# Performance work log

Measured on AMD Instinct MI355X. Metric: run time of the kernel, lower is better.

Reference implementation:

```python
import jax, jax.numpy as jnp
import numpy as np

B, S, D, H = 2, 2048, 1024, 16
DEPTH = D // H


def setup_inputs() -> dict:
    key = jax.random.key(0)
    ks = jax.random.split(key, 8)
    w_scale = 0.02
    # causal mask: 1.0 where attention is NOT allowed (added as mask * -1e9)
    causal = jnp.triu(jnp.ones((S, S), dtype=jnp.float32), k=1)[None, None]  # [1,1,S,S]
    return {
        "q": jax.random.normal(ks[0], (B, S, D), dtype=jnp.float32),
        "k": jax.random.normal(ks[1], (B, S, D), dtype=jnp.float32),
        "v": jax.random.normal(ks[2], (B, S, D), dtype=jnp.float32),
        "mask": causal,
        "Wq": jax.random.normal(ks[3], (D, D), dtype=jnp.float32) * w_scale,
        "bq": jnp.zeros((D,), dtype=jnp.float32),
        "Wk": jax.random.normal(ks[4], (D, D), dtype=jnp.float32) * w_scale,
        "bk": jnp.zeros((D,), dtype=jnp.float32),
        "Wv": jax.random.normal(ks[5], (D, D), dtype=jnp.float32) * w_scale,
        "bv": jnp.zeros((D,), dtype=jnp.float32),
        "Wo": jax.random.normal(ks[6], (D, D), dtype=jnp.float32) * w_scale,
        "bo": jnp.zeros((D,), dtype=jnp.float32),
    }


def _split_heads(x):
    # [B,S,D] -> [B,H,S,depth]
    return x.reshape(B, S, H, DEPTH).transpose(0, 2, 1, 3)


def reference(q, k, v, mask, Wq, bq, Wk, bk, Wv, bv, Wo, bo):
    qh = _split_heads(q @ Wq + bq)
    kh = _split_heads(k @ Wk + bk)
    vh = _split_heads(v @ Wv + bv)
    scale = 1.0 / jnp.sqrt(jnp.asarray(DEPTH, dtype=qh.dtype))
    logits = jnp.einsum('bhqd,bhkd->bhqk', qh, kh) * scale  # [B,H,S,S]
    logits = logits + mask * (-1e9)
    attn = jax.nn.softmax(logits, axis=-1)
    out = jnp.einsum('bhqk,bhkd->bhqd', attn, vh)  # [B,H,S,depth]
    out = out.transpose(0, 2, 1, 3).reshape(B, S, D)
    return out @ Wo + bo
```

## Files before the change

### kernel.cpp

```cpp
#include <hip/hip_runtime.h>


typedef unsigned short u16;
typedef unsigned int u32;

using bf16x8 = __attribute__((ext_vector_type(8))) short;
using bf16x4 = __attribute__((ext_vector_type(4))) short;
using f32x4  = __attribute__((ext_vector_type(4))) float;

#define SEQ 2048
#define DMODEL 1024
#define NHEAD 16
#define DEPTH 64
#define BATCH 2
#define M_ROWS (BATCH * SEQ)

__device__ __forceinline__ u16 f2bf(float f) {
    union { float f; u32 u; } v; v.f = f;
    u32 u = v.u;
    return (u16)((u + 0x7FFFu + ((u >> 16) & 1u)) >> 16);
}
__device__ __forceinline__ u16 f2bf_trunc(float f) {
    union { float f; u32 u; } v; v.f = f;
    return (u16)(v.u >> 16);
}

__device__ __forceinline__ f32x4 mfma16(bf16x8 a, bf16x8 b, f32x4 c) {
    return __builtin_amdgcn_mfma_f32_16x16x32_bf16(a, b, c, 0, 0, 0);
}

__device__ __forceinline__ void glds16(const u16* src, u16* dst) {
    __builtin_amdgcn_global_load_lds((const __attribute__((address_space(1))) void*)src,
                                     (__attribute__((address_space(3))) void*)dst,
                                     16, 0, 0);
}

__device__ __forceinline__ bf16x8 fragld(const u16* base, int lr, int gc) {
    return *(const bf16x8*)(base + lr * 64 + (((gc ^ lr) & 7) << 3));
}
__device__ __forceinline__ bf16x8 fragld32(const u16* base, int lr, int gc) {
    return *(const bf16x8*)(base + lr * 32 + (((gc ^ lr) & 3) << 3));
}

__global__ void cvt3_kernel(const float* __restrict__ q, const float* __restrict__ k,
                            const float* __restrict__ v,
                            u16* __restrict__ qo, u16* __restrict__ ko, u16* __restrict__ vo) {
    const float* in; u16* out;
    if (blockIdx.z == 0)      { in = q; out = qo; }
    else if (blockIdx.z == 1) { in = k; out = ko; }
    else                      { in = v; out = vo; }
    int idx = blockIdx.x * blockDim.x + threadIdx.x;
    float4 val = ((const float4*)in)[idx];
    ushort4 o;
    o.x = f2bf(val.x); o.y = f2bf(val.y); o.z = f2bf(val.z); o.w = f2bf(val.w);
    ((ushort4*)out)[idx] = o;
}

__global__ void wtrans_kernel(const float* __restrict__ Wq, const float* __restrict__ Wk,
                              const float* __restrict__ Wv, const float* __restrict__ Wo,
                              u16* __restrict__ Wqt, u16* __restrict__ Wkt,
                              u16* __restrict__ Wvt, u16* __restrict__ Wot) {
    __shared__ float tile[32][33];
    const float* W; u16* Wt;
    switch (blockIdx.z) {
        case 0: W = Wq; Wt = Wqt; break;
        case 1: W = Wk; Wt = Wkt; break;
        case 2: W = Wv; Wt = Wvt; break;
        default: W = Wo; Wt = Wot; break;
    }
    int k0 = blockIdx.x * 32, n0 = blockIdx.y * 32;
    int tx = threadIdx.x, ty = threadIdx.y;
#pragma unroll
    for (int i = 0; i < 4; ++i)
        tile[ty + 8 * i][tx] = W[(size_t)(k0 + ty + 8 * i) * DMODEL + n0 + tx];
    __syncthreads();
#pragma unroll
    for (int i = 0; i < 4; ++i)
        Wt[(size_t)(n0 + ty + 8 * i) * DMODEL + k0 + tx] = f2bf(tile[tx][ty + 8 * i]);
}

template<int TM>
__device__ __forceinline__ void gemm_core(const u16* __restrict__ A, const u16* __restrict__ Bt,
                                          const float* __restrict__ bias,
                                          u16* __restrict__ outb, float* __restrict__ outf,
                                          int mode, float oscale, int bm0, int bn0) {
    constexpr int K = DMODEL;
    constexpr int NT = K / 32;
    constexpr int MI = TM / 32;
    constexpr int ACH = TM / 64;
    __shared__ u16 As[2][TM * 32];
    __shared__ u16 Bs[2][128 * 32];
    int t = threadIdx.x;
    int w = t >> 6, lane = t & 63, l15 = lane & 15, quad = lane >> 4;
    int wm = (w >> 1) * (TM / 2), wn = (w & 1) * 64;
    int r16 = lane >> 2, g4 = lane & 3;
    int gswz = ((g4 ^ (r16 & 3)) << 3);
    f32x4 acc[MI][4] = {};

#define QSTAGE(p, kt) do { \
    _Pragma("unroll") for (int c = 0; c < ACH; ++c) { \
        int ch = w * ACH + c; \
        glds16(A + (size_t)(bm0 + ch * 16 + r16) * K + (kt) * 32 + gswz, &As[p][ch * 512]); } \
    _Pragma("unroll") for (int c = 0; c < 2; ++c) { \
        int ch = w * 2 + c; \
        glds16(Bt + (size_t)(bn0 + ch * 16 + r16) * K + (kt) * 32 + gswz, &Bs[p][ch * 512]); } \
    } while (0)

    QSTAGE(0, 0);
    __syncthreads();

    for (int kt = 0; kt < NT; ++kt) {
        int cur = kt & 1;
        if (kt + 1 < NT) QSTAGE(cur ^ 1, kt + 1);
        bf16x8 af[MI], bfr[4];
#pragma unroll
        for (int i = 0; i < MI; ++i) af[i]  = fragld32(&As[cur][0], wm + i * 16 + l15, quad);
#pragma unroll
        for (int j = 0; j < 4;  ++j) bfr[j] = fragld32(&Bs[cur][0], wn + j * 16 + l15, quad);
#pragma unroll
        for (int i = 0; i < MI; ++i)
#pragma unroll
            for (int j = 0; j < 4; ++j)
                acc[i][j] = mfma16(af[i], bfr[j], acc[i][j]);
        __syncthreads();
    }
#undef QSTAGE

#pragma unroll
    for (int i = 0; i < MI; ++i) {
        int row_g0 = bm0 + wm + i * 16 + quad * 4;
#pragma unroll
        for (int j = 0; j < 4; ++j) {
            int col_g = bn0 + wn + j * 16 + l15;
            float bsv = bias[col_g];
#pragma unroll
            for (int r = 0; r < 4; ++r) {
                float v = (acc[i][j][r] + bsv) * oscale;
                int rg = row_g0 + r;
                if (mode == 2) {
                    outf[(size_t)rg * DMODEL + col_g] = v;
                } else {
                    int b = rg >> 11, s = rg & (SEQ - 1);
                    int h = col_g >> 6, d = col_g & 63;
                    size_t idx;
                    if (mode == 0) idx = ((size_t)(b * NHEAD + h) * SEQ + s) * DEPTH + d;
                    else           idx = ((size_t)(b * NHEAD + h) * DEPTH + d) * SEQ + s;
                    outb[idx] = f2bf(v);
                }
            }
        }
    }
}

#define SCALE_Q 0.1803368801111204f

__global__ __launch_bounds__(256, 4) void gemm_qkv(
        const u16* __restrict__ qb, const u16* __restrict__ kb, const u16* __restrict__ vb,
        const u16* __restrict__ Wqt, const u16* __restrict__ Wkt, const u16* __restrict__ Wvt,
        const float* __restrict__ bq, const float* __restrict__ bk, const float* __restrict__ bv,
        u16* __restrict__ Qp, u16* __restrict__ Kp, u16* __restrict__ Vpt) {
    int id = blockIdx.x;
    int c = id & 7, m = id >> 3;
    int slab = c * 12 + (m >> 3);
    int x = m & 7;
    int z = slab >> 5, y = slab & 31;
    int bm0 = y * 128, bn0 = x * 128;
    if (z == 0)      gemm_core<128>(qb, Wqt, bq, Qp,  nullptr, 0, SCALE_Q, bm0, bn0);
    else if (z == 1) gemm_core<128>(kb, Wkt, bk, Kp,  nullptr, 0, 1.0f,    bm0, bn0);
    else             gemm_core<128>(vb, Wvt, bv, Vpt, nullptr, 1, 1.0f,    bm0, bn0);
}

__global__ __launch_bounds__(256, 4) void gemm_out(
        const u16* __restrict__ attnb, const u16* __restrict__ Wot,
        const float* __restrict__ bo, float* __restrict__ out) {
    int id = blockIdx.x;
    int c = id & 7, m = id >> 3;
    int slab = c * 8 + (m >> 3);
    int x = m & 7;
    gemm_core<64>(attnb, Wot, bo, nullptr, out, 2, 1.0f, slab * 64, x * 128);
}

#define LP 72
__global__ __launch_bounds__(256) void attn_kernel(
        const u16* __restrict__ Qp, const u16* __restrict__ Kp,
        const u16* __restrict__ Vpt, u16* __restrict__ attn_out, u32* __restrict__ ctrs) {
    __shared__ u16 Klds[2][64 * 64];
    __shared__ u16 Vtlds[2][64 * 64];
    __shared__ u16 Plds[4 * 16 * LP];
    __shared__ u32 item_s;
    int t = threadIdx.x, w = t >> 6, lane = t & 63, l15 = lane & 15, quad = lane >> 4;
    int r8 = lane >> 3, g8 = lane & 7;
    int gswz = ((g8 ^ r8) << 3);
    u16* Pw = Plds + w * 16 * LP;
    int xcd = blockIdx.x & 7;
    u32* my_ctr = ctrs + xcd * 32;

    bf16x8 ones;
#pragma unroll
    for (int i = 0; i < 8; ++i) ones[i] = (short)0x3F80;

    for (;;) {
        if (t == 0) item_s = atomicAdd(my_ctr, 1);
        __syncthreads();
        u32 item = item_s;
        if (item >= 128) break;
        int qt = 31 - (int)(item >> 2);
        int bh = xcd * 4 + (int)(item & 3);
        int q0 = qt * 64;
        int nkt = qt + 1;
        int b = bh >> 4, h = bh & 15;
        const u16* Qbase = Qp  + (size_t)bh * SEQ * DEPTH;
        const u16* Kbase = Kp  + (size_t)bh * SEQ * DEPTH;
        const u16* Vbase = Vpt + (size_t)bh * DEPTH * SEQ;

        int qrow = q0 + w * 16 + l15;
        bf16x8 qf[2];
        qf[0] = *(const bf16x8*)(Qbase + (size_t)qrow * DEPTH + quad * 8);
        qf[1] = *(const bf16x8*)(Qbase + (size_t)qrow * DEPTH + 32 + quad * 8);

        f32x4 of[4] = {};
        f32x4 lacc = {};

#pragma unroll
        for (int c2 = 0; c2 < 2; ++c2) {
            int ch = w * 2 + c2;
            glds16(Kbase + (size_t)(ch * 8 + r8) * DEPTH + gswz, Klds[0] + ch * 512);
            glds16(Vbase + (size_t)(ch * 8 + r8) * SEQ + gswz,   Vtlds[0] + ch * 512);
        }

        for (int kt = 0; kt < nkt; ++kt) {
            int cur = kt & 1;
            __syncthreads();
            if (kt + 1 < nkt) {
                int nx = cur ^ 1, kn = kt + 1;
#pragma unroll
                for (int c2 = 0; c2 < 2; ++c2) {
                    int ch = w * 2 + c2;
                    glds16(Kbase + (size_t)(kn * 64 + ch * 8 + r8) * DEPTH + gswz,
                           Klds[nx] + ch * 512);
                    glds16(Vbase + (size_t)(ch * 8 + r8) * SEQ + kn * 64 + gswz,
                           Vtlds[nx] + ch * 512);
                }
            }
            f32x4 st[4] = {};
#pragma unroll
            for (int nt = 0; nt < 4; ++nt)
#pragma unroll
                for (int kk = 0; kk < 2; ++kk)
                    st[nt] = mfma16(fragld(Klds[cur], nt * 16 + l15, kk * 4 + quad), qf[kk], st[nt]);

            bool diag = (kt == nkt - 1);
            int qlv = w * 16 + l15;
#pragma unroll
            for (int nt = 0; nt < 4; ++nt) {
                bf16x4 pv;
#pragma unroll
                for (int r = 0; r < 4; ++r) {
                    float e = exp2f(st[nt][r]);
                    if (diag) {
                        int keyl = nt * 16 + quad * 4 + r;
                        e = (keyl > qlv) ? 0.f : e;
                    }
                    pv[r] = (short)f2bf_trunc(e);
                }
                *(bf16x4*)(Pw + l15 * LP + nt * 16 + quad * 4) = pv;
            }
            asm volatile("" ::: "memory");
            bf16x8 pf[2];
            pf[0] = *(const bf16x8*)(Pw + l15 * LP + quad * 8);
            pf[1] = *(const bf16x8*)(Pw + l15 * LP + 32 + quad * 8);
#pragma unroll
            for (int kk = 0; kk < 2; ++kk) {
                lacc = mfma16(pf[kk], ones, lacc);
#pragma unroll
                for (int nt = 0; nt < 4; ++nt)
                    of[nt] = mfma16(pf[kk], fragld(Vtlds[cur], nt * 16 + l15, kk * 4 + quad), of[nt]);
            }
        }
#pragma unroll
        for (int r = 0; r < 4; ++r) {
            float inv = 1.0f / lacc[r];
            int s_ = q0 + w * 16 + quad * 4 + r;
#pragma unroll
            for (int nt = 0; nt < 4; ++nt) {
                int dcol = h * DEPTH + nt * 16 + l15;
                attn_out[((size_t)(b * SEQ + s_)) * DMODEL + dcol] = f2bf(of[nt][r] * inv);
            }
        }
    }
}

extern "C" void kernel_launch(void* const* d_in, const int* in_sizes, int n_in,
                              void* d_out, int out_size, void* d_ws, size_t ws_size,
                              hipStream_t stream) {
    const float* q  = (const float*)d_in[0];
    const float* k  = (const float*)d_in[1];
    const float* v  = (const float*)d_in[2];
    const float* Wq = (const float*)d_in[4];
    const float* bq = (const float*)d_in[5];
    const float* Wk = (const float*)d_in[6];
    const float* bk = (const float*)d_in[7];
    const float* Wv = (const float*)d_in[8];
    const float* bv = (const float*)d_in[9];
    const float* Wo = (const float*)d_in[10];
    const float* bo = (const float*)d_in[11];
    float* out = (float*)d_out;

    char* ws = (char*)d_ws;
    const size_t SZ_ACT = (size_t)M_ROWS * DMODEL * 2;
    const size_t SZ_W   = (size_t)DMODEL * DMODEL * 2;
    u16* qb   = (u16*)(ws);
    u16* kb   = (u16*)(ws + SZ_ACT);
    u16* vb   = (u16*)(ws + 2 * SZ_ACT);
    u16* Wqt  = (u16*)(ws + 3 * SZ_ACT);
    u16* Wkt  = (u16*)(ws + 3 * SZ_ACT + SZ_W);
    u16* Wvt  = (u16*)(ws + 3 * SZ_ACT + 2 * SZ_W);
    u16* Wot  = (u16*)(ws + 3 * SZ_ACT + 3 * SZ_W);
    u16* Qp   = (u16*)(ws + 3 * SZ_ACT + 4 * SZ_W);
    u16* Kp   = (u16*)(ws + 4 * SZ_ACT + 4 * SZ_W);
    u16* Vpt  = (u16*)(ws + 5 * SZ_ACT + 4 * SZ_W);
    u16* attnb= (u16*)(ws + 6 * SZ_ACT + 4 * SZ_W);
    u32* ctrs = (u32*)(ws + 7 * SZ_ACT + 4 * SZ_W);

    hipMemsetAsync(ctrs, 0, 1024, stream);
    cvt3_kernel<<<dim3(4096, 1, 3), 256, 0, stream>>>(q, k, v, qb, kb, vb);
    wtrans_kernel<<<dim3(32, 32, 4), dim3(32, 8), 0, stream>>>(Wq, Wk, Wv, Wo, Wqt, Wkt, Wvt, Wot);
    gemm_qkv<<<dim3(768), 256, 0, stream>>>(
        qb, kb, vb, Wqt, Wkt, Wvt, bq, bk, bv, Qp, Kp, Vpt);
    attn_kernel<<<dim3(768), 256, 0, stream>>>(Qp, Kp, Vpt, attnb, ctrs);
    gemm_out<<<dim3(512), 256, 0, stream>>>(attnb, Wot, bo, out);
}
```

Baseline: 227.3 us.

## Process 32 query rows per wave in attention to reuse K/V fragments

The attention block drops from four waves to two, and each wave now handles two 16-row query groups. Each K and V fragment loaded from LDS therefore feeds two MFMAs, halving LDS fragment reads per unit of compute. Each thread now issues four async K/V chunk loads instead of two. The cost is more accumulator registers per wave and fewer waves per block for hiding latency, though more blocks can be resident at once.

```diff
diff --git a/kernel.cpp b/kernel.cpp
--- a/kernel.cpp
+++ b/kernel.cpp
@@ -181,17 +181,17 @@
 }
 
 #define LP 72
-__global__ __launch_bounds__(256) void attn_kernel(
+__global__ __launch_bounds__(128) void attn_kernel(
         const u16* __restrict__ Qp, const u16* __restrict__ Kp,
         const u16* __restrict__ Vpt, u16* __restrict__ attn_out, u32* __restrict__ ctrs) {
     __shared__ u16 Klds[2][64 * 64];
     __shared__ u16 Vtlds[2][64 * 64];
-    __shared__ u16 Plds[4 * 16 * LP];
+    __shared__ u16 Plds[2 * 32 * LP];
     __shared__ u32 item_s;
     int t = threadIdx.x, w = t >> 6, lane = t & 63, l15 = lane & 15, quad = lane >> 4;
     int r8 = lane >> 3, g8 = lane & 7;
     int gswz = ((g8 ^ r8) << 3);
-    u16* Pw = Plds + w * 16 * LP;
+    u16* Pw = Plds + w * 32 * LP;
     int xcd = blockIdx.x & 7;
     u32* my_ctr = ctrs + xcd * 32;
 
@@ -213,17 +213,20 @@
         const u16* Kbase = Kp  + (size_t)bh * SEQ * DEPTH;
         const u16* Vbase = Vpt + (size_t)bh * DEPTH * SEQ;
 
-        int qrow = q0 + w * 16 + l15;
-        bf16x8 qf[2];
-        qf[0] = *(const bf16x8*)(Qbase + (size_t)qrow * DEPTH + quad * 8);
-        qf[1] = *(const bf16x8*)(Qbase + (size_t)qrow * DEPTH + 32 + quad * 8);
-
-        f32x4 of[4] = {};
-        f32x4 lacc = {};
-
-#pragma unroll
-        for (int c2 = 0; c2 < 2; ++c2) {
-            int ch = w * 2 + c2;
+        bf16x8 qf[2][2];
+#pragma unroll
+        for (int g = 0; g < 2; ++g) {
+            int qrow = q0 + w * 32 + g * 16 + l15;
+            qf[g][0] = *(const bf16x8*)(Qbase + (size_t)qrow * DEPTH + quad * 8);
+            qf[g][1] = *(const bf16x8*)(Qbase + (size_t)qrow * DEPTH + 32 + quad * 8);
+        }
+
+        f32x4 of[2][4] = {};
+        f32x4 lacc[2] = {};
+
+#pragma unroll
+        for (int c2 = 0; c2 < 4; ++c2) {
+            int ch = w * 4 + c2;
             glds16(Kbase + (size_t)(ch * 8 + r8) * DEPTH + gswz, Klds[0] + ch * 512);
             glds16(Vbase + (size_t)(ch * 8 + r8) * SEQ + gswz,   Vtlds[0] + ch * 512);
         }
@@ -234,59 +237,74 @@
             if (kt + 1 < nkt) {
                 int nx = cur ^ 1, kn = kt + 1;
 #pragma unroll
-                for (int c2 = 0; c2 < 2; ++c2) {
-                    int ch = w * 2 + c2;
+                for (int c2 = 0; c2 < 4; ++c2) {
+                    int ch = w * 4 + c2;
                     glds16(Kbase + (size_t)(kn * 64 + ch * 8 + r8) * DEPTH + gswz,
                            Klds[nx] + ch * 512);
                     glds16(Vbase + (size_t)(ch * 8 + r8) * SEQ + kn * 64 + gswz,
                            Vtlds[nx] + ch * 512);
                 }
             }
-            f32x4 st[4] = {};
+            f32x4 st[2][4] = {};
 #pragma unroll
             for (int nt = 0; nt < 4; ++nt)
 #pragma unroll
-                for (int kk = 0; kk < 2; ++kk)
-                    st[nt] = mfma16(fragld(Klds[cur], nt * 16 + l15, kk * 4 + quad), qf[kk], st[nt]);
+                for (int kk = 0; kk < 2; ++kk) {
+                    bf16x8 kf = fragld(Klds[cur], nt * 16 + l15, kk * 4 + quad);
+                    st[0][nt] = mfma16(kf, qf[0][kk], st[0][nt]);
+                    st[1][nt] = mfma16(kf, qf[1][kk], st[1][nt]);
+                }
 
             bool diag = (kt == nkt - 1);
-            int qlv = w * 16 + l15;
-#pragma unroll
-            for (int nt = 0; nt < 4; ++nt) {
-                bf16x4 pv;
-#pragma unroll
-                for (int r = 0; r < 4; ++r) {
-                    float e = exp2f(st[nt][r]);
-                    if (diag) {
-                        int keyl = nt * 16 + quad * 4 + r;
-                        e = (keyl > qlv) ? 0.f : e;
+#pragma unroll
+            for (int g = 0; g < 2; ++g) {
+                int qlv = w * 32 + g * 16 + l15;
+#pragma unroll
+                for (int nt = 0; nt < 4; ++nt) {
+                    bf16x4 pv;
+#pragma unroll
+                    for (int r = 0; r < 4; ++r) {
+                        float e = exp2f(st[g][nt][r]);
+                        if (diag) {
+                            int keyl = nt * 16 + quad * 4 + r;
+                            e = (keyl > qlv) ? 0.f : e;
+                        }
+                        pv[r] = (short)f2bf_trunc(e);
                     }
-                    pv[r] = (short)f2bf_trunc(e);
-                }
-                *(bf16x4*)(Pw + l15 * LP + nt * 16 + quad * 4) = pv;
+                    *(bf16x4*)(Pw + (g * 16 + l15) * LP + nt * 16 + quad * 4) = pv;
+                }
             }
             asm volatile("" ::: "memory");
-            bf16x8 pf[2];
-            pf[0] = *(const bf16x8*)(Pw + l15 * LP + quad * 8);
-            pf[1] = *(const bf16x8*)(Pw + l15 * LP + 32 + quad * 8);
+            bf16x8 pf[2][2];
+#pragma unroll
+            for (int g = 0; g < 2; ++g) {
+                pf[g][0] = *(const bf16x8*)(Pw + (g * 16 + l15) * LP + quad * 8);
+                pf[g][1] = *(const bf16x8*)(Pw + (g * 16 + l15) * LP + 32 + quad * 8);
+            }
 #pragma unroll
             for (int kk = 0; kk < 2; ++kk) {
-                lacc = mfma16(pf[kk], ones, lacc);
-#pragma unroll
-                for (int nt = 0; nt < 4; ++nt)
-                    of[nt] = mfma16(pf[kk], fragld(Vtlds[cur], nt * 16 + l15, kk * 4 + quad), of[nt]);
+                lacc[0] = mfma16(pf[0][kk], ones, lacc[0]);
+                lacc[1] = mfma16(pf[1][kk], ones, lacc[1]);
+#pragma unroll
+                for (int nt = 0; nt < 4; ++nt) {
+                    bf16x8 vf = fragld(Vtlds[cur], nt * 16 + l15, kk * 4 + quad);
+                    of[0][nt] = mfma16(pf[0][kk], vf, of[0][nt]);
+                    of[1][nt] = mfma16(pf[1][kk], vf, of[1][nt]);
+                }
             }
         }
 #pragma unroll
-        for (int r = 0; r < 4; ++r) {
-            float inv = 1.0f / lacc[r];
-            int s_ = q0 + w * 16 + quad * 4 + r;
-#pragma unroll
-            for (int nt = 0; nt < 4; ++nt) {
-                int dcol = h * DEPTH + nt * 16 + l15;
-                attn_out[((size_t)(b * SEQ + s_)) * DMODEL + dcol] = f2bf(of[nt][r] * inv);
-            }
-        }
+        for (int g = 0; g < 2; ++g)
+#pragma unroll
+            for (int r = 0; r < 4; ++r) {
+                float inv = 1.0f / lacc[g][r];
+                int s_ = q0 + w * 32 + g * 16 + quad * 4 + r;
+#pragma unroll
+                for (int nt = 0; nt < 4; ++nt) {
+                    int dcol = h * DEPTH + nt * 16 + l15;
+                    attn_out[((size_t)(b * SEQ + s_)) * DMODEL + dcol] = f2bf(of[g][nt][r] * inv);
+                }
+            }
     }
 }
 
@@ -327,6 +345,6 @@
     wtrans_kernel<<<dim3(32, 32, 4), dim3(32, 8), 0, stream>>>(Wq, Wk, Wv, Wo, Wqt, Wkt, Wvt, Wot);
     gemm_qkv<<<dim3(768), 256, 0, stream>>>(
         qb, kb, vb, Wqt, Wkt, Wvt, bq, bk, bv, Qp, Kp, Vpt);
-    attn_kernel<<<dim3(768), 256, 0, stream>>>(Qp, Kp, Vpt, attnb, ctrs);
+    attn_kernel<<<dim3(768), 128, 0, stream>>>(Qp, Kp, Vpt, attnb, ctrs);
     gemm_out<<<dim3(512), 256, 0, stream>>>(attnb, Wot, bo, out);
 }
```

Measured after the change: 239.3 us. +5.3%, slower.
